# Performance work log

Hardware: AMD Instinct MI355X
Metric: run time of the kernel (lower is better)

## Reference

```python
import jax, jax.numpy as jnp
import numpy as np

D = 512       # input_embedding_dimensions
H = 2         # num_heads
HD = D // H   # head_dim = 256
B = 16
S = 1194      # max_sequence_length


def setup_inputs() -> dict:
    key = jax.random.key(0)
    k1, k2, k3, k4, k5 = jax.random.split(key, 5)
    scale_in = 1.0 / np.sqrt(D)
    return {
        "positional_embeddings": jax.random.normal(k1, (B, S, D), dtype=jnp.float32),
        "W_qkv": jax.random.uniform(k2, (D, 3 * D), minval=-scale_in, maxval=scale_in, dtype=jnp.float32),
        "b_qkv": jax.random.uniform(k3, (3 * D,), minval=-scale_in, maxval=scale_in, dtype=jnp.float32),
        "W_out": jax.random.uniform(k4, (D, D), minval=-scale_in, maxval=scale_in, dtype=jnp.float32),
        "b_out": jax.random.uniform(k5, (D,), minval=-scale_in, maxval=scale_in, dtype=jnp.float32),
    }


def reference(positional_embeddings, W_qkv, b_qkv, W_out, b_out):
    x = positional_embeddings              # [B, S, D]
    b, s, _ = x.shape
    qkv = x @ W_qkv + b_qkv                # [B, S, 3D]
    q, k, v = jnp.split(qkv, 3, axis=-1)

    def split_heads(t):
        return t.reshape(b, s, H, HD).transpose(0, 2, 1, 3)  # [B, H, S, HD]

    q, k, v = split_heads(q), split_heads(k), split_heads(v)
    scores = jnp.einsum("bhqd,bhkd->bhqk", q, k) / jnp.sqrt(jnp.float32(HD))
    causal = jnp.tril(jnp.ones((s, s), dtype=bool))          # [S, S]
    scores = jnp.where(causal[None, None, :, :], scores, -jnp.inf)
    att = jax.nn.softmax(scores, axis=-1)                    # [B, H, S, S]
    out = jnp.einsum("bhqk,bhkd->bhqd", att, v)              # [B, H, S, HD]
    out = out.transpose(0, 2, 1, 3).reshape(b, s, D)         # [B, S, D]
    return out @ W_out + b_out
```

## Files before the change

kernel.cpp:

```cpp
#include <hip/hip_runtime.h>
#include <stdint.h>

#define D_    512
#define H_    2
#define HD_   256
#define B_    16
#define S_    1194
#define MTOK  19104
#define MPAD  19200
#define SPAD  1216
#define NQKV  1536
#define NKT   38
#define LOG2E 1.44269504088896340736f

typedef unsigned short u16;
typedef unsigned int u32;
typedef __attribute__((ext_vector_type(8))) short bf16x8;
typedef __attribute__((ext_vector_type(4))) float f32x4;

__device__ inline u16 f2bf(float x) {
  union { float f; unsigned u; } c; c.f = x;
  unsigned r = c.u + 0x7fffu + ((c.u >> 16) & 1u);
  return (u16)(r >> 16);
}

__device__ inline void async_copy16(void* lds, const void* g) {
  __builtin_amdgcn_global_load_lds(
      (__attribute__((address_space(1))) void*)(g),
      (__attribute__((address_space(3))) void*)(lds),
      16, 0, 0);
}

__global__ void convert_kernel(const float* __restrict__ X,
                               const float* __restrict__ Wqkv,
                               const float* __restrict__ Wout,
                               u16* __restrict__ Xf,
                               u16* __restrict__ Wqf,
                               u16* __restrict__ Wof) {
  const int NXG = MPAD * 64;
  const int NQG = 12 * 8 * 16 * 64;
  const int NOG = 4 * 8 * 16 * 64;
  const int TOT = NXG + NQG + NOG;
  int stride = gridDim.x * blockDim.x;
  for (int g = blockIdx.x * blockDim.x + threadIdx.x; g < TOT; g += stride) {
    if (g < NXG) {
      int lane = g & 63, f = (g >> 6) & 15, kt = (g >> 10) & 7, mt = g >> 13;
      int i = mt * 128 + (f & 7) * 16 + (lane & 15);
      int k = kt * 64 + (f >> 3) * 32 + (lane >> 4) * 8;
      bf16x8 o;
      if (i < MTOK) {
        f32x4 v0 = *(const f32x4*)&X[(size_t)i * 512 + k];
        f32x4 v1 = *(const f32x4*)&X[(size_t)i * 512 + k + 4];
#pragma unroll
        for (int e = 0; e < 4; ++e) { o[e] = (short)f2bf(v0[e]); o[4 + e] = (short)f2bf(v1[e]); }
      } else {
#pragma unroll
        for (int e = 0; e < 8; ++e) o[e] = 0;
      }
      *(bf16x8*)&Xf[(size_t)g * 8] = o;
    } else if (g < NXG + NQG) {
      int gg = g - NXG;
      int lane = gg & 63, f = (gg >> 6) & 15, kt = (gg >> 10) & 7, nt = gg >> 13;
      int j = nt * 128 + (f & 7) * 16 + (lane & 15);
      int k = kt * 64 + (f >> 3) * 32 + (lane >> 4) * 8;
      bf16x8 o;
#pragma unroll
      for (int e = 0; e < 8; ++e) o[e] = (short)f2bf(Wqkv[(size_t)(k + e) * NQKV + j]);
      *(bf16x8*)&Wqf[(size_t)gg * 8] = o;
    } else {
      int gg = g - NXG - NQG;
      int lane = gg & 63, f = (gg >> 6) & 15, kt = (gg >> 10) & 7, nt = gg >> 13;
      int j = nt * 128 + (f & 7) * 16 + (lane & 15);
      int k = kt * 64 + (f >> 3) * 32 + (lane >> 4) * 8;
      bf16x8 o;
#pragma unroll
      for (int e = 0; e < 8; ++e) o[e] = (short)f2bf(Wout[(size_t)(k + e) * 512 + j]);
      *(bf16x8*)&Wof[(size_t)gg * 8] = o;
    }
  }
}

template<int MODE>
__global__ __launch_bounds__(256, 2) void gemm_kernel(
    const u16* __restrict__ Af, const u16* __restrict__ Bf,
    const float* __restrict__ bias, int nb,
    u16* __restrict__ Qb, u16* __restrict__ Kf, u16* __restrict__ Vf,
    float* __restrict__ Cout)
{
  __shared__ u16 ldsA[16 * 512];
  __shared__ u16 ldsB[16 * 512];

  const int t  = threadIdx.x;
  const int l  = t & 63;
  const int w  = t >> 6;
  const int lr = l >> 4, lc = l & 15;

  const int nwg = gridDim.x;
  const int qq = nwg >> 3, rr8 = nwg & 7;
  const int xcd = blockIdx.x & 7, off = blockIdx.x >> 3;
  const int wgid = (xcd < rr8 ? xcd * (qq + 1) : rr8 * (qq + 1) + (xcd - rr8) * qq) + off;
  const int m0 = (wgid / nb) * 128;
  const int n0 = (wgid % nb) * 128;
  const bool vband = (MODE == 0) && ((wgid % nb) >= 8);

  const u16* pA = Af + ((size_t)(m0 >> 7) * 128 + w) * 512 + l * 8;
  const u16* pB = Bf + ((size_t)(n0 >> 7) * 128 + w) * 512 + l * 8;

  f32x4 acc[4][4] = {};

  for (int kt = 0; kt < 8; ++kt) {
    __syncthreads();
    const u16* qA = pA + kt * 8192;
    const u16* qB = pB + kt * 8192;
#pragma unroll
    for (int c = 0; c < 4; ++c) {
      async_copy16(&ldsA[(c * 4 + w) * 512], qA + c * 2048);
      async_copy16(&ldsB[(c * 4 + w) * 512], qB + c * 2048);
    }
    __syncthreads();
#pragma unroll
    for (int kk = 0; kk < 2; ++kk) {
      bf16x8 af[4], bfr[4];
#pragma unroll
      for (int m = 0; m < 4; ++m)
        af[m] = *(bf16x8*)&ldsA[((kk * 8 + (w >> 1) * 4 + m) * 64 + l) * 8];
#pragma unroll
      for (int n = 0; n < 4; ++n)
        bfr[n] = *(bf16x8*)&ldsB[((kk * 8 + (w & 1) * 4 + n) * 64 + l) * 8];
      __builtin_amdgcn_s_setprio(1);
      if (!vband) {
#pragma unroll
        for (int m = 0; m < 4; ++m)
#pragma unroll
          for (int n = 0; n < 4; ++n)
            acc[m][n] = __builtin_amdgcn_mfma_f32_16x16x32_bf16(bfr[n], af[m], acc[m][n], 0, 0, 0);
      } else {
#pragma unroll
        for (int m = 0; m < 4; ++m)
#pragma unroll
          for (int n = 0; n < 4; ++n)
            acc[m][n] = __builtin_amdgcn_mfma_f32_16x16x32_bf16(af[m], bfr[n], acc[m][n], 0, 0, 0);
      }
      __builtin_amdgcn_s_setprio(0);
    }
  }

  if (MODE == 1) {
#pragma unroll
    for (int m = 0; m < 4; ++m) {
      int i = m0 + (w >> 1) * 64 + m * 16 + lc;
      if (i >= MTOK) continue;
#pragma unroll
      for (int n = 0; n < 4; ++n) {
        int jb = n0 + (w & 1) * 64 + n * 16 + lr * 4;
        f32x4 bv = *(const f32x4*)&bias[jb];
        f32x4 o;
#pragma unroll
        for (int r = 0; r < 4; ++r) o[r] = acc[m][n][r] + bv[r];
        *(f32x4*)&Cout[(size_t)i * D_ + jb] = o;
      }
    }
  } else if (!vband) {
#pragma unroll
    for (int m = 0; m < 4; ++m) {
      int i = m0 + (w >> 1) * 64 + m * 16 + lc;
      if (i >= MTOK) continue;
      int b = i / S_, s = i - b * S_;
      int stK = s >> 5, nfs = (s >> 4) & 1, lisK = s & 15;
#pragma unroll
      for (int n = 0; n < 4; ++n) {
        int jb = n0 + (w & 1) * 64 + n * 16 + lr * 4;
        f32x4 bv = *(const f32x4*)&bias[jb];
        uint64_t pk = 0;
#pragma unroll
        for (int r = 0; r < 4; ++r)
          pk |= (uint64_t)f2bf(acc[m][n][r] + bv[r]) << (16 * r);
        int which = jb >> 9, h = (jb >> 8) & 1, d = jb & 255;
        int bh = b * H_ + h;
        if (which == 0) {
          *(uint64_t*)&Qb[(size_t)(bh * SPAD + s) * HD_ + d] = pk;
        } else {
          *(uint64_t*)&Kf[(((size_t)(bh * NKT + stK)) * 16 + (d >> 5) * 2 + nfs) * 512 +
                          (((d >> 3) & 3) * 16 + lisK) * 8 + (d & 7)] = pk;
        }
      }
    }
  } else {
    int jv[4]; float bj[4];
#pragma unroll
    for (int n = 0; n < 4; ++n) { jv[n] = n0 + (w & 1) * 64 + n * 16 + lc; bj[n] = bias[jv[n]]; }
#pragma unroll
    for (int m = 0; m < 4; ++m) {
#pragma unroll
      for (int rp = 0; rp < 4; rp += 2) {
        int i0 = m0 + (w >> 1) * 64 + m * 16 + lr * 4 + rp;
        if (i0 >= MTOK) continue;
        int b = i0 / S_, s = i0 - b * S_;
        int stK = s >> 5, lvhi = (s >> 3) & 3, es = s & 7;
#pragma unroll
        for (int n = 0; n < 4; ++n) {
          int j = jv[n];
          int h = (j >> 8) & 1, d = j & 255;
          int bh = b * H_ + h;
          u32 pk = (u32)f2bf(acc[m][n][rp] + bj[n]) |
                   ((u32)f2bf(acc[m][n][rp + 1] + bj[n]) << 16);
          *(u32*)&Vf[(((size_t)(bh * NKT + stK)) * 16 + (d >> 4)) * 512 +
                     (lvhi * 16 + (d & 15)) * 8 + es] = pk;
        }
      }
    }
  }
}

__global__ __launch_bounds__(256, 2) void attn_kernel(
    const u16* __restrict__ Qb, const u16* __restrict__ Kf,
    const u16* __restrict__ Vf, u16* __restrict__ Obf)
{
  __shared__ u16 ldsK[2][16 * 512];
  __shared__ u16 ldsP[4][16 * 36];

  const int id   = blockIdx.x;
  const int xcd  = id & 7;
  const int slot = id >> 3;
  const int bh   = xcd + 8 * (slot / 19);
  const int qt   = 18 - (slot % 19);
  const int q0   = qt * 64;
  const int nkv  = 2 * qt + 2;
  const int t  = threadIdx.x, l = t & 63, w = t >> 6;
  const int lr = l >> 4, lc = l & 15;
  const int wq0 = q0 + w * 16;
  const int qrow_l = wq0 + lc;

  bf16x8 qf[8];
  const u16* qbase = Qb + (size_t)(bh * SPAD + qrow_l) * HD_ + lr * 8;
#pragma unroll
  for (int kb = 0; kb < 8; ++kb)
    qf[kb] = *(const bf16x8*)(qbase + kb * 32);

  f32x4 oacc[16] = {};
  float mrow = -1e30f, lsum = 0.f;

  const u16* kroot = Kf + ((size_t)(bh * NKT) * 16 + w) * 512 + l * 8;
  const u16* vroot = Vf + ((size_t)(bh * NKT) * 16) * 512 + l * 8;

#pragma unroll
  for (int c = 0; c < 4; ++c) {
    async_copy16(&ldsK[0][(c * 4 + w) * 512], kroot + c * 2048);
    async_copy16(&ldsK[1][(c * 4 + w) * 512], kroot + 8192 + c * 2048);
  }
  bf16x8 vfr[16];
#pragma unroll
  for (int f = 0; f < 16; ++f) vfr[f] = *(const bf16x8*)(vroot + f * 512);
  __syncthreads();

  f32x4 saccA[2] = {}, saccB[2] = {};
  __builtin_amdgcn_s_setprio(1);
#pragma unroll
  for (int kb = 0; kb < 8; ++kb)
#pragma unroll
    for (int nf = 0; nf < 2; ++nf) {
      bf16x8 kf = *(bf16x8*)&ldsK[0][((kb * 2 + nf) * 64 + l) * 8];
      saccA[nf] = __builtin_amdgcn_mfma_f32_16x16x32_bf16(kf, qf[kb], saccA[nf], 0, 0, 0);
    }
  __builtin_amdgcn_s_setprio(0);
  __syncthreads();

#define SUBITER(J, S, N)                                                       \
  {                                                                            \
    const int j_ = (J);                                                        \
    if (j_ + 2 < nkv) {                                                        \
      const u16* kb_ = kroot + (size_t)(j_ + 2) * 8192;                        \
      _Pragma("unroll")                                                        \
      for (int c = 0; c < 4; ++c)                                              \
        async_copy16(&ldsK[j_ & 1][(c * 4 + w) * 512], kb_ + c * 2048);        \
    }                                                                          \
    const int kv0 = j_ * 32;                                                   \
    float sv[2][4];                                                            \
    float pm = -1e30f;                                                         \
    if (kv0 + 31 <= wq0) {                                                     \
      _Pragma("unroll")                                                        \
      for (int nf = 0; nf < 2; ++nf)                                           \
        _Pragma("unroll")                                                      \
        for (int r = 0; r < 4; ++r) {                                          \
          float v = S[nf][r] * 0.0625f;                                        \
          sv[nf][r] = v;                                                       \
          pm = fmaxf(pm, v);                                                   \
        }                                                                      \
    } else {                                                                   \
      _Pragma("unroll")                                                        \
      for (int nf = 0; nf < 2; ++nf)                                           \
        _Pragma("unroll")                                                      \
        for (int r = 0; r < 4; ++r) {                                          \
          int kvi = kv0 + nf * 16 + lr * 4 + r;                                \
          float v = ((kvi <= qrow_l) && (kvi < S_)) ? S[nf][r] * 0.0625f       \
                                                    : -1e30f;                  \
          sv[nf][r] = v;                                                       \
          pm = fmaxf(pm, v);                                                   \
        }                                                                      \
    }                                                                          \
    pm = fmaxf(pm, __shfl_xor(pm, 16));                                        \
    pm = fmaxf(pm, __shfl_xor(pm, 32));                                        \
    bool skip = (pm <= mrow + 8.0f);                                           \
    if (!__all(skip)) {                                                        \
      float mn = fmaxf(mrow, pm);                                              \
      float sc = exp2f((mrow - mn) * LOG2E);                                   \
      mrow = mn;                                                               \
      lsum *= sc;                                                              \
      _Pragma("unroll")                                                        \
      for (int nf = 0; nf < 16; ++nf)                                          \
        _Pragma("unroll")                                                      \
        for (int r = 0; r < 4; ++r) oacc[nf][r] *= sc;                         \
    }                                                                          \
    _Pragma("unroll")                                                          \
    for (int nf = 0; nf < 2; ++nf) {                                           \
      float p0 = exp2f((sv[nf][0] - mrow) * LOG2E);                            \
      float p1 = exp2f((sv[nf][1] - mrow) * LOG2E);                            \
      float p2 = exp2f((sv[nf][2] - mrow) * LOG2E);                            \
      float p3 = exp2f((sv[nf][3] - mrow) * LOG2E);                            \
      lsum += (p0 + p1) + (p2 + p3);                                           \
      uint64_t pk = (uint64_t)f2bf(p0) | ((uint64_t)f2bf(p1) << 16) |          \
                    ((uint64_t)f2bf(p2) << 32) | ((uint64_t)f2bf(p3) << 48);   \
      *(uint64_t*)&ldsP[w][lc * 36 + nf * 16 + lr * 4] = pk;                   \
    }                                                                          \
    if (j_ + 1 < nkv) {                                                        \
      N[0] = (f32x4){0.f, 0.f, 0.f, 0.f};                                      \
      N[1] = (f32x4){0.f, 0.f, 0.f, 0.f};                                      \
      __builtin_amdgcn_s_setprio(1);                                           \
      _Pragma("unroll")                                                        \
      for (int kb = 0; kb < 8; ++kb)                                           \
        _Pragma("unroll")                                                      \
        for (int nf = 0; nf < 2; ++nf) {                                       \
          bf16x8 kf =                                                          \
              *(bf16x8*)&ldsK[(j_ + 1) & 1][((kb * 2 + nf) * 64 + l) * 8];     \
          N[nf] = __builtin_amdgcn_mfma_f32_16x16x32_bf16(kf, qf[kb], N[nf],   \
                                                          0, 0, 0);            \
        }                                                                      \
      __builtin_amdgcn_s_setprio(0);                                           \
    }                                                                          \
    __syncthreads();                                                           \
    bf16x8 pf = *(bf16x8*)&ldsP[w][lc * 36 + lr * 8];                          \
    __builtin_amdgcn_s_setprio(1);                                             \
    _Pragma("unroll")                                                          \
    for (int nf = 0; nf < 16; ++nf)                                            \
      oacc[nf] =                                                               \
          __builtin_amdgcn_mfma_f32_16x16x32_bf16(vfr[nf], pf, oacc[nf],       \
                                                  0, 0, 0);                    \
    __builtin_amdgcn_s_setprio(0);                                             \
    if (j_ + 1 < nkv) {                                                        \
      const u16* vb_ = vroot + (size_t)(j_ + 1) * 8192;                        \
      _Pragma("unroll")                                                        \
      for (int f = 0; f < 16; ++f) vfr[f] = *(const bf16x8*)(vb_ + f * 512);   \
    }                                                                          \
  }

  for (int kt = 0; kt < nkv; kt += 2) {
    SUBITER(kt, saccA, saccB);
    SUBITER(kt + 1, saccB, saccA);
  }
#undef SUBITER

  float s = lsum;
  s += __shfl_xor(s, 16);
  s += __shfl_xor(s, 32);
  float inv = 1.0f / s;

  const int b = bh >> 1, h = bh & 1;
  if (qrow_l < S_) {
    int i = b * S_ + qrow_l;
    int it = i >> 7, mf = (i >> 4) & 7, li = i & 15;
#pragma unroll
    for (int nf = 0; nf < 16; ++nf) {
      int j0 = h * HD_ + nf * 16 + lr * 4;
      uint64_t pk = 0;
#pragma unroll
      for (int r = 0; r < 4; ++r)
        pk |= (uint64_t)f2bf(oacc[nf][r] * inv) << (16 * r);
      size_t addr = (((size_t)(it * 8 + (j0 >> 6))) * 16 + ((j0 >> 5) & 1) * 8 + mf) * 512 +
                    (((j0 >> 3) & 3) * 16 + li) * 8 + (j0 & 7);
      *(uint64_t*)&Obf[addr] = pk;
    }
  }
}

extern "C" void kernel_launch(void* const* d_in, const int* in_sizes, int n_in,
                              void* d_out, int out_size, void* d_ws, size_t ws_size,
                              hipStream_t stream) {
  const float* X    = (const float*)d_in[0];
  const float* Wqkv = (const float*)d_in[1];
  const float* bqkv = (const float*)d_in[2];
  const float* Wout = (const float*)d_in[3];
  const float* bout = (const float*)d_in[4];
  float* out = (float*)d_out;

  char* ws = (char*)d_ws;
  u16* Xf  = (u16*)ws;  ws += (size_t)MPAD * D_ * 2;
  u16* Wqf = (u16*)ws;  ws += (size_t)NQKV * D_ * 2;
  u16* Wof = (u16*)ws;  ws += (size_t)D_ * D_ * 2;
  u16* Qb  = (u16*)ws;  ws += (size_t)B_ * H_ * SPAD * HD_ * 2;
  u16* Kf  = (u16*)ws;  ws += (size_t)B_ * H_ * SPAD * HD_ * 2;
  u16* Vf  = (u16*)ws;  ws += (size_t)B_ * H_ * SPAD * HD_ * 2;
  u16* Obf = (u16*)ws;  ws += (size_t)MPAD * D_ * 2;

  convert_kernel<<<2048, 256, 0, stream>>>(X, Wqkv, Wout, Xf, Wqf, Wof);
  gemm_kernel<0><<<1800, 256, 0, stream>>>(Xf, Wqf, bqkv, 12, Qb, Kf, Vf, nullptr);
  attn_kernel<<<608, 256, 0, stream>>>(Qb, Kf, Vf, Obf);
  gemm_kernel<1><<<600, 256, 0, stream>>>(Obf, Wof, bout, 4, nullptr, nullptr, nullptr, out);
}
```

Measured before the change: 146.9 us.

## Split long causal attention query tiles across two KV halves with combine kernel

Query tiles 10-18 now have their KV range split into two halves, each handled by its own block. Each half writes unnormalized partial outputs plus per-row max and sum, and a new combine kernel merges the halves with a log-sum-exp rescale. This replaces a 608-block grid that had heavily imbalanced causal work with 896 more even blocks. The cost is an extra kernel launch, extra traffic for the partial buffers (which reuse the Xf and Wqf workspace), and bf16 rounding of the unnormalized partials.

```diff
diff --git a/kernel.cpp b/kernel.cpp
--- a/kernel.cpp
+++ b/kernel.cpp
@@ -11,6 +11,9 @@
 #define SPAD  1216
 #define NQKV  1536
 #define NKT   38
+#define QSPLIT 10
+#define NSQT  9
+#define NSROW 18432
 #define LOG2E 1.44269504088896340736f
 
 typedef unsigned short u16;
@@ -22,6 +25,9 @@
   union { float f; unsigned u; } c; c.f = x;
   unsigned r = c.u + 0x7fffu + ((c.u >> 16) & 1u);
   return (u16)(r >> 16);
+}
+__device__ inline float bf2f(u16 v) {
+  union { unsigned u; float f; } c; c.u = ((u32)v) << 16; return c.f;
 }
 
 __device__ inline void async_copy16(void* lds, const void* g) {
@@ -214,7 +220,8 @@
 
 __global__ __launch_bounds__(256, 2) void attn_kernel(
     const u16* __restrict__ Qb, const u16* __restrict__ Kf,
-    const u16* __restrict__ Vf, u16* __restrict__ Obf)
+    const u16* __restrict__ Vf, u16* __restrict__ Obf,
+    u16* __restrict__ Opart, float* __restrict__ ML)
 {
   __shared__ u16 ldsK[2][16 * 512];
   __shared__ u16 ldsP[4][16 * 36];
@@ -222,10 +229,23 @@
   const int id   = blockIdx.x;
   const int xcd  = id & 7;
   const int slot = id >> 3;
-  const int bh   = xcd + 8 * (slot / 19);
-  const int qt   = 18 - (slot % 19);
-  const int q0   = qt * 64;
-  const int nkv  = 2 * qt + 2;
+  const int bh   = xcd + 8 * (slot / 28);
+  const int u    = slot % 28;
+  int qt, half, st0, endk;
+  if (u < 18) {
+    qt   = 18 - (u >> 1);
+    half = u & 1;
+    int nkv = 2 * qt + 2;
+    int lo  = (qt + 2) & ~1;
+    st0  = half ? lo : 0;
+    endk = half ? nkv : lo;
+  } else {
+    qt   = 9 - (u - 18);
+    half = -1;
+    st0  = 0;
+    endk = 2 * qt + 2;
+  }
+  const int q0 = qt * 64;
   const int t  = threadIdx.x, l = t & 63, w = t >> 6;
   const int lr = l >> 4, lc = l & 15;
   const int wq0 = q0 + w * 16;
@@ -245,12 +265,13 @@
 
 #pragma unroll
   for (int c = 0; c < 4; ++c) {
-    async_copy16(&ldsK[0][(c * 4 + w) * 512], kroot + c * 2048);
-    async_copy16(&ldsK[1][(c * 4 + w) * 512], kroot + 8192 + c * 2048);
+    async_copy16(&ldsK[0][(c * 4 + w) * 512], kroot + (size_t)st0 * 8192 + c * 2048);
+    async_copy16(&ldsK[1][(c * 4 + w) * 512], kroot + (size_t)(st0 + 1) * 8192 + c * 2048);
   }
   bf16x8 vfr[16];
 #pragma unroll
-  for (int f = 0; f < 16; ++f) vfr[f] = *(const bf16x8*)(vroot + f * 512);
+  for (int f = 0; f < 16; ++f)
+    vfr[f] = *(const bf16x8*)(vroot + (size_t)st0 * 8192 + f * 512);
   __syncthreads();
 
   f32x4 saccA[2] = {}, saccB[2] = {};
@@ -268,7 +289,7 @@
 #define SUBITER(J, S, N)                                                       \
   {                                                                            \
     const int j_ = (J);                                                        \
-    if (j_ + 2 < nkv) {                                                        \
+    if (j_ + 2 < endk) {                                                       \
       const u16* kb_ = kroot + (size_t)(j_ + 2) * 8192;                        \
       _Pragma("unroll")                                                        \
       for (int c = 0; c < 4; ++c)                                              \
@@ -322,7 +343,7 @@
                     ((uint64_t)f2bf(p2) << 32) | ((uint64_t)f2bf(p3) << 48);   \
       *(uint64_t*)&ldsP[w][lc * 36 + nf * 16 + lr * 4] = pk;                   \
     }                                                                          \
-    if (j_ + 1 < nkv) {                                                        \
+    if (j_ + 1 < endk) {                                                       \
       N[0] = (f32x4){0.f, 0.f, 0.f, 0.f};                                      \
       N[1] = (f32x4){0.f, 0.f, 0.f, 0.f};                                      \
       __builtin_amdgcn_s_setprio(1);                                           \
@@ -346,14 +367,14 @@
           __builtin_amdgcn_mfma_f32_16x16x32_bf16(vfr[nf], pf, oacc[nf],       \
                                                   0, 0, 0);                    \
     __builtin_amdgcn_s_setprio(0);                                             \
-    if (j_ + 1 < nkv) {                                                        \
+    if (j_ + 1 < endk) {                                                       \
       const u16* vb_ = vroot + (size_t)(j_ + 1) * 8192;                        \
       _Pragma("unroll")                                                        \
       for (int f = 0; f < 16; ++f) vfr[f] = *(const bf16x8*)(vb_ + f * 512);   \
     }                                                                          \
   }
 
-  for (int kt = 0; kt < nkv; kt += 2) {
+  for (int kt = st0; kt < endk; kt += 2) {
     SUBITER(kt, saccA, saccB);
     SUBITER(kt + 1, saccB, saccA);
   }
@@ -362,24 +383,76 @@
   float s = lsum;
   s += __shfl_xor(s, 16);
   s += __shfl_xor(s, 32);
-  float inv = 1.0f / s;
-
-  const int b = bh >> 1, h = bh & 1;
-  if (qrow_l < S_) {
-    int i = b * S_ + qrow_l;
-    int it = i >> 7, mf = (i >> 4) & 7, li = i & 15;
+
+  if (half < 0) {
+    float inv = 1.0f / s;
+    const int b = bh >> 1, h = bh & 1;
+    if (qrow_l < S_) {
+      int i = b * S_ + qrow_l;
+      int it = i >> 7, mf = (i >> 4) & 7, li = i & 15;
+#pragma unroll
+      for (int nf = 0; nf < 16; ++nf) {
+        int j0 = h * HD_ + nf * 16 + lr * 4;
+        uint64_t pk = 0;
+#pragma unroll
+        for (int r = 0; r < 4; ++r)
+          pk |= (uint64_t)f2bf(oacc[nf][r] * inv) << (16 * r);
+        size_t addr = (((size_t)(it * 8 + (j0 >> 6))) * 16 + ((j0 >> 5) & 1) * 8 + mf) * 512 +
+                      (((j0 >> 3) & 3) * 16 + li) * 8 + (j0 & 7);
+        *(uint64_t*)&Obf[addr] = pk;
+      }
+    }
+  } else {
+    int rowl = ((bh * NSQT) + (qt - QSPLIT)) * 64 + w * 16 + lc;
+    size_t robase = ((size_t)(half ? NSROW : 0) + rowl) * 256;
 #pragma unroll
     for (int nf = 0; nf < 16; ++nf) {
-      int j0 = h * HD_ + nf * 16 + lr * 4;
       uint64_t pk = 0;
 #pragma unroll
       for (int r = 0; r < 4; ++r)
-        pk |= (uint64_t)f2bf(oacc[nf][r] * inv) << (16 * r);
-      size_t addr = (((size_t)(it * 8 + (j0 >> 6))) * 16 + ((j0 >> 5) & 1) * 8 + mf) * 512 +
-                    (((j0 >> 3) & 3) * 16 + li) * 8 + (j0 & 7);
-      *(uint64_t*)&Obf[addr] = pk;
-    }
-  }
+        pk |= (uint64_t)f2bf(oacc[nf][r]) << (16 * r);
+      *(uint64_t*)&Opart[robase + nf * 16 + lr * 4] = pk;
+    }
+    if (l < 16) {
+      int rml = ((bh * NSQT) + (qt - QSPLIT)) * 64 + w * 16 + l;
+      ML[(((half ? NSROW : 0) + rml)) * 2]     = mrow;
+      ML[(((half ? NSROW : 0) + rml)) * 2 + 1] = s;
+    }
+  }
+}
+
+__global__ void combine_kernel(const u16* __restrict__ Opart,
+                               const float* __restrict__ ML,
+                               u16* __restrict__ Obf) {
+  int g = blockIdx.x * 256 + threadIdx.x;
+  if (g >= NSROW * 32) return;
+  int row = g >> 5, dg = g & 31;
+  int bh = row / (NSQT * 64), rem = row % (NSQT * 64);
+  int qt = QSPLIT + rem / 64, qr = rem & 63;
+  int qrow = qt * 64 + qr;
+  if (qrow >= S_) return;
+
+  float m1 = ML[row * 2],           l1 = ML[row * 2 + 1];
+  float m2 = ML[(NSROW + row) * 2], l2 = ML[(NSROW + row) * 2 + 1];
+  float m  = fmaxf(m1, m2);
+  float a1 = exp2f((m1 - m) * LOG2E);
+  float a2 = exp2f((m2 - m) * LOG2E);
+  float inv = 1.0f / (a1 * l1 + a2 * l2);
+
+  bf16x8 o1 = *(const bf16x8*)&Opart[((size_t)row) * 256 + dg * 8];
+  bf16x8 o2 = *(const bf16x8*)&Opart[((size_t)(NSROW + row)) * 256 + dg * 8];
+  bf16x8 o;
+#pragma unroll
+  for (int e = 0; e < 8; ++e)
+    o[e] = (short)f2bf((a1 * bf2f((u16)o1[e]) + a2 * bf2f((u16)o2[e])) * inv);
+
+  int b = bh >> 1, h = bh & 1;
+  int i = b * S_ + qrow;
+  int j0 = h * HD_ + dg * 8;
+  int it = i >> 7, mf = (i >> 4) & 7, li = i & 15;
+  size_t addr = (((size_t)(it * 8 + (j0 >> 6))) * 16 + ((j0 >> 5) & 1) * 8 + mf) * 512 +
+                (((j0 >> 3) & 3) * 16 + li) * 8;
+  *(bf16x8*)&Obf[addr] = o;
 }
 
 extern "C" void kernel_launch(void* const* d_in, const int* in_sizes, int n_in,
@@ -400,9 +473,12 @@
   u16* Kf  = (u16*)ws;  ws += (size_t)B_ * H_ * SPAD * HD_ * 2;
   u16* Vf  = (u16*)ws;  ws += (size_t)B_ * H_ * SPAD * HD_ * 2;
   u16* Obf = (u16*)ws;  ws += (size_t)MPAD * D_ * 2;
+  u16*   Opart = Xf;
+  float* MLb   = (float*)Wqf;
 
   convert_kernel<<<2048, 256, 0, stream>>>(X, Wqkv, Wout, Xf, Wqf, Wof);
   gemm_kernel<0><<<1800, 256, 0, stream>>>(Xf, Wqf, bqkv, 12, Qb, Kf, Vf, nullptr);
-  attn_kernel<<<608, 256, 0, stream>>>(Qb, Kf, Vf, Obf);
+  attn_kernel<<<896, 256, 0, stream>>>(Qb, Kf, Vf, Obf, Opart, MLb);
+  combine_kernel<<<(NSROW * 32 + 255) / 256, 256, 0, stream>>>(Opart, MLb, Obf);
   gemm_kernel<1><<<600, 256, 0, stream>>>(Obf, Wof, bout, 4, nullptr, nullptr, nullptr, out);
 }
```

Measured after the change: 157.1 us. +6.9%, slower.
